# Optimization experiments

Hardware: AMD Instinct MI355X
Metric: run time of the kernel (lower is better)

## Reference

```python
import jax, jax.numpy as jnp
import numpy as np
from jax import lax

S, D, T, FT, FP, H, NH = 100, 30, 40, 512, 3, 64, 4
DH = H // NH

PARAM_SHAPES = {
    'pg_Wih': (S, 3 * H, FP), 'pg_Whh': (S, 3 * H, H), 'pg_bih': (S, 3 * H), 'pg_bhh': (S, 3 * H),
    'pa_W': (S, H, H), 'pa_b': (S, H),
    'tl_Wall': (S, 4 * H, FT), 'tl_bWall': (S, 4 * H), 'tl_Uall': (S, 4 * H, H), 'tl_bUall': (S, 4 * H),
    'tl_Wd': (S, H, H), 'tl_bd': (S, H),
    'ta_W': (S, H, H), 'ta_b': (S, H),
    'sg_Wih': (S, 3 * H, H), 'sg_Whh': (S, 3 * H, H), 'sg_bih': (S, 3 * H), 'sg_bhh': (S, 3 * H),
    'sa_W': (S, H, H), 'sa_b': (S, H),
    'bi_W': (S, H, H, H), 'bi_b': (S, H),
    'bl_W': (S, 2, H), 'bl_b': (S, 2),
    'mha_Wq': (H, H), 'mha_bq': (H,), 'mha_Wk': (H, H), 'mha_bk': (H,),
    'fc_W': (2, H), 'fc_b': (2,),
}


def setup_inputs() -> dict:
    key = jax.random.key(0)
    ks = jax.random.split(key, len(PARAM_SHAPES) + 5)
    inp = {}
    for (name, shp), k in zip(PARAM_SHAPES.items(), ks[:len(PARAM_SHAPES)]):
        inp[name] = jax.random.normal(k, shp, dtype=jnp.float32) * 0.05
    k0, k1, k2, k3, k4 = ks[len(PARAM_SHAPES):]
    inp['text_input'] = jax.random.normal(k0, (S, D, T, FT), dtype=jnp.float32)
    inp['price_input'] = jax.random.normal(k1, (S, D, FP), dtype=jnp.float32)
    inp['timestamps'] = jax.random.uniform(k2, (S, D, T), dtype=jnp.float32)
    inp['label'] = jax.random.randint(k3, (S,), 0, 2, dtype=jnp.int32)
    inp['adj'] = jax.random.randint(k4, (S, S), 0, 2, dtype=jnp.int32)
    inp['train'] = 0
    return inp


def _gru(x_seq, Wih, Whh, bih, bhh):
    # x_seq: [T, Din] -> outs [T, H], h_last [H]
    h0 = jnp.zeros((Whh.shape[1],), x_seq.dtype)
    def step(h, x):
        gx = Wih @ x + bih
        gh = Whh @ h + bhh
        xr, xz, xn = jnp.split(gx, 3)
        hr, hz, hn = jnp.split(gh, 3)
        r = jax.nn.sigmoid(xr + hr)
        z = jax.nn.sigmoid(xz + hz)
        n = jnp.tanh(xn + r * hn)
        h2 = (1.0 - z) * n + z * h
        return h2, h2
    h_last, outs = lax.scan(step, h0, x_seq)
    return outs, h_last


def _timelstm(x_seq, ts, Wall, bWall, Uall, bUall, Wd, bd):
    # x_seq: [T, FT], ts: [T] -> outs [T, H], h_last [H]
    h0 = jnp.zeros((Wd.shape[0],), x_seq.dtype)
    def step(carry, xt):
        h, c = carry
        x, t = xt
        c_s1 = jnp.tanh(Wd @ c + bd)
        c_adj = c - c_s1 + c_s1 * t  # time-decayed cell, as in source
        g = Uall @ h + bUall + Wall @ x + bWall
        f, i, o, ct = jnp.split(g, 4)
        f = jax.nn.sigmoid(f)
        i = jax.nn.sigmoid(i)
        o = jax.nn.sigmoid(o)
        ct = jax.nn.sigmoid(ct)  # sigmoid (not tanh), faithful to source
        c2 = f * c_adj + i * ct
        h2 = o * jnp.tanh(c2)
        return (h2, c2), h2
    (h, c), outs = lax.scan(step, (h0, h0), (x_seq, ts))
    return outs, h


def _attn(outs, h, W, b):
    # Luong-style attention pooling over time: scores_t = outs_t . (W h + b)
    scores = outs @ (W @ h + b)
    return jax.nn.softmax(scores) @ outs


def _stock(price, text, ts, pg_Wih, pg_Whh, pg_bih, pg_bhh, pa_W, pa_b,
           tl_Wall, tl_bWall, tl_Uall, tl_bUall, tl_Wd, tl_bd, ta_W, ta_b,
           sg_Wih, sg_Whh, sg_bih, sg_bhh, sa_W, sa_b, bi_W, bi_b):
    p_outs, p_h = _gru(price, pg_Wih, pg_Whh, pg_bih, pg_bhh)
    x = _attn(p_outs, p_h, pa_W, pa_b)  # [H] price vector
    def day(txt_d, ts_d):
        o, hh = _timelstm(txt_d, ts_d, tl_Wall, tl_bWall, tl_Uall, tl_bUall, tl_Wd, tl_bd)
        return _attn(o, hh, ta_W, ta_b)
    news = jax.vmap(day)(text, ts)  # [D, H]
    s_outs, s_h = _gru(news, sg_Wih, sg_Whh, sg_bih, sg_bhh)
    tvec = _attn(s_outs, s_h, sa_W, sa_b)  # [H] text vector
    return jnp.tanh(jnp.einsum('i,kij,j->k', tvec, bi_W, x) + bi_b)


def _forward(text_input, price_input, timestamps,
             pg_Wih, pg_Whh, pg_bih, pg_bhh, pa_W, pa_b,
             tl_Wall, tl_bWall, tl_Uall, tl_bUall, tl_Wd, tl_bd, ta_W, ta_b,
             sg_Wih, sg_Whh, sg_bih, sg_bhh, sa_W, sa_b, bi_W, bi_b,
             bl_W, bl_b, mha_Wq, mha_bq, mha_Wk, mha_bk, fc_W, fc_b, label):
    feature = jax.vmap(_stock)(price_input, text_input, timestamps,
                               pg_Wih, pg_Whh, pg_bih, pg_bhh, pa_W, pa_b,
                               tl_Wall, tl_bWall, tl_Uall, tl_bUall, tl_Wd, tl_bd, ta_W, ta_b,
                               sg_Wih, sg_Whh, sg_bih, sg_bhh, sa_W, sa_b, bi_W, bi_b)  # [S, H]
    # source bug kept: blending uses the LAST stock's layer on all stocks
    out_1 = jnp.tanh(feature @ bl_W[-1].T + bl_b[-1])  # [S, 2]
    # multi-head self-attention over the stock axis (dropout off: eval mode)
    Q = (feature @ mha_Wq.T + mha_bq).reshape(S, NH, DH)
    K = (feature @ mha_Wk.T + mha_bk).reshape(S, NH, DH)
    V = feature.reshape(S, NH, DH)
    scores = jnp.einsum('shd,thd->hst', Q, K) / (DH ** 0.5)
    a = jax.nn.softmax(scores, axis=-1)
    mh = jnp.einsum('hst,thd->shd', a, V).reshape(S, H)
    x = jax.nn.elu(mh @ fc_W.T + fc_b)  # [S, 2]
    output = jax.nn.softmax(x + out_1, axis=1)
    # faithful to source: CrossEntropyLoss applied to already-softmaxed output
    logp = jax.nn.log_softmax(output, axis=1)
    loss = -jnp.mean(jnp.take_along_axis(logp, label[:, None].astype(jnp.int32), axis=1))
    return loss, output


def reference(text_input, price_input, timestamps,
              pg_Wih, pg_Whh, pg_bih, pg_bhh, pa_W, pa_b,
              tl_Wall, tl_bWall, tl_Uall, tl_bUall, tl_Wd, tl_bd, ta_W, ta_b,
              sg_Wih, sg_Whh, sg_bih, sg_bhh, sa_W, sa_b, bi_W, bi_b,
              bl_W, bl_b, mha_Wq, mha_bq, mha_Wk, mha_bk, fc_W, fc_b,
              label, adj, train):
    del adj, train  # adj feeds dead GraphAttentionLayer in source; eval-mode dropout is identity
    return _forward(text_input, price_input, timestamps,
                    pg_Wih, pg_Whh, pg_bih, pg_bhh, pa_W, pa_b,
                    tl_Wall, tl_bWall, tl_Uall, tl_bUall, tl_Wd, tl_bd, ta_W, ta_b,
                    sg_Wih, sg_Whh, sg_bih, sg_bhh, sa_W, sa_b, bi_W, bi_b,
                    bl_W, bl_b, mha_Wq, mha_bq, mha_Wk, mha_bk, fc_W, fc_b, label)
```

## Files before the change

kernel.cpp:

```cpp
#include <hip/hip_runtime.h>
#include <math.h>

#define S_  100
#define D_  30
#define T_  40
#define FT_ 512
#define FP_ 3
#define H_  64
#define G3  192
#define G4  256
#define M_  (D_*T_)
#define NDY 6

typedef __attribute__((ext_vector_type(8))) short short8_t;
typedef __attribute__((ext_vector_type(4))) short short4_t;
typedef __attribute__((ext_vector_type(4))) float f32x4;

__device__ __forceinline__ float sigm(float x){ return 1.0f/(1.0f+__expf(-x)); }
__device__ __forceinline__ float tanhfast(float x){
  float e = __expf(2.0f*x);
  return 1.0f - 2.0f/(e + 1.0f);
}
__device__ __forceinline__ short f2bf(float f){
  unsigned u = __builtin_bit_cast(unsigned, f);
  u += 0x7FFFu + ((u>>16)&1u);
  return (short)(u>>16);
}
__device__ __forceinline__ float bf2f(unsigned short u){
  unsigned x = ((unsigned)u) << 16;
  return __builtin_bit_cast(float, x);
}
__device__ __forceinline__ short8_t pack8(float4 a, float4 b){
  short8_t o;
  o[0]=f2bf(a.x); o[1]=f2bf(a.y); o[2]=f2bf(a.z); o[3]=f2bf(a.w);
  o[4]=f2bf(b.x); o[5]=f2bf(b.y); o[6]=f2bf(b.z); o[7]=f2bf(b.w);
  return o;
}

__global__ __launch_bounds__(512, 2) void k_gemm_price(
    const float* __restrict__ text, const float* __restrict__ Wall,
    const float* __restrict__ bW, const float* __restrict__ bU,
    unsigned short* __restrict__ GX,
    const float* __restrict__ price, const float* __restrict__ pWih,
    const float* __restrict__ pWhh, const float* __restrict__ pbih,
    const float* __restrict__ pbhh, const float* __restrict__ paW,
    const float* __restrict__ pab, float* __restrict__ xvec)
{
  __shared__ __align__(16) char smem[78848];
  const int tid = threadIdx.x;

  if (blockIdx.x < 1000) {
    const int orig = blockIdx.x;
    const int wg = (orig & 7) * 125 + (orig >> 3);
    const int s  = wg / 10;
    const int mb = wg % 10;
    const int m0 = mb * 128;
    const int lane = tid & 63, wave = tid >> 6;
    const int wm = wave >> 2, wn = wave & 3;
    const int fr = lane & 15, fk = (lane >> 4) * 8;

    float (*As)[128][36] = (float(*)[128][36])smem;
    short (*Bs)[G4][40]  = (short(*)[G4][40])(smem + 36864);
    short (*Es)[264]     = (short(*)[264])smem;
    float* biasL         = (float*)(smem + 77824);

    if (tid < G4) biasL[tid] = bW[s*G4 + tid] + bU[s*G4 + tid];

    const float* X   = text + (size_t)s * ((size_t)M_*FT_);
    const float* Wsl = Wall + (size_t)s * ((size_t)G4*FT_);

    const int rowA = tid >> 2;
    const int colA = (tid & 3) * 8;
    int ar = m0 + rowA; if (ar > M_-1) ar = M_-1;
    const float* aSrc = X + (size_t)ar*FT_ + colA;
    const int rowB = tid >> 1;
    const int colB = (tid & 1) * 16;
    const float* bSrc = Wsl + (size_t)rowB*FT_ + colB;

    f32x4 acc[4][4];
    #pragma unroll
    for (int i=0;i<4;++i)
      #pragma unroll
      for (int j=0;j<4;++j) acc[i][j] = (f32x4)(0.f);

    float4 la0, la1, lb0, lb1, lb2, lb3;
    la0 = *reinterpret_cast<const float4*>(aSrc);
    la1 = *reinterpret_cast<const float4*>(aSrc + 4);
    lb0 = *reinterpret_cast<const float4*>(bSrc);
    lb1 = *reinterpret_cast<const float4*>(bSrc + 4);
    lb2 = *reinterpret_cast<const float4*>(bSrc + 8);
    lb3 = *reinterpret_cast<const float4*>(bSrc + 12);

    for (int kp = 0; kp < 16; ++kp) {
      const int buf = kp & 1;
      *reinterpret_cast<float4*>(&As[buf][rowA][colA])     = la0;
      *reinterpret_cast<float4*>(&As[buf][rowA][colA + 4]) = la1;
      *reinterpret_cast<short8_t*>(&Bs[buf][rowB][colB])     = pack8(lb0, lb1);
      *reinterpret_cast<short8_t*>(&Bs[buf][rowB][colB + 8]) = pack8(lb2, lb3);
      __syncthreads();
      if (kp + 1 < 16) {
        const int ko = (kp + 1) * 32;
        la0 = *reinterpret_cast<const float4*>(aSrc + ko);
        la1 = *reinterpret_cast<const float4*>(aSrc + ko + 4);
        lb0 = *reinterpret_cast<const float4*>(bSrc + ko);
        lb1 = *reinterpret_cast<const float4*>(bSrc + ko + 4);
        lb2 = *reinterpret_cast<const float4*>(bSrc + ko + 8);
        lb3 = *reinterpret_cast<const float4*>(bSrc + ko + 12);
      }
      short8_t bfr[4];
      #pragma unroll
      for (int nt = 0; nt < 4; ++nt)
        bfr[nt] = *reinterpret_cast<const short8_t*>(&Bs[buf][wn*64 + nt*16 + fr][fk]);
      #pragma unroll
      for (int mt = 0; mt < 4; ++mt) {
        float4 x = *reinterpret_cast<const float4*>(&As[buf][wm*64 + mt*16 + fr][fk]);
        float4 y = *reinterpret_cast<const float4*>(&As[buf][wm*64 + mt*16 + fr][fk + 4]);
        short8_t afr = pack8(x, y);
        #pragma unroll
        for (int nt = 0; nt < 4; ++nt)
          acc[mt][nt] = __builtin_amdgcn_mfma_f32_16x16x32_bf16(afr, bfr[nt], acc[mt][nt], 0,0,0);
      }
    }

    __syncthreads();
    {
      const int cl = lane & 15, rh = (lane >> 4) * 4;
      #pragma unroll
      for (int mt = 0; mt < 4; ++mt)
        #pragma unroll
        for (int nt = 0; nt < 4; ++nt) {
          const int cc = wn*64 + nt*16 + cl;
          const float b = biasL[cc];
          #pragma unroll
          for (int r = 0; r < 4; ++r)
            Es[wm*64 + mt*16 + rh + r][cc] = f2bf(acc[mt][nt][r] + b);
        }
    }
    __syncthreads();
    {
      const int r = tid >> 2;
      const int c0 = (tid & 3) * 64;
      const int m = m0 + r;
      if (m < M_) {
        unsigned short* dst = GX + ((size_t)s*M_ + m)*G4 + c0;
        #pragma unroll
        for (int j = 0; j < 8; ++j)
          *reinterpret_cast<short8_t*>(dst + j*8) =
              *reinterpret_cast<const short8_t*>(&Es[r][c0 + j*8]);
      }
    }
    return;
  }

  {
    const int s = blockIdx.x - 1000;
    float* hs   = (float*)smem;
    float (*outsb)[H_+1] = (float(*)[H_+1])(hs + 64);
    float* gsum = hs + 64 + D_*(H_+1);
    float* gxn  = gsum + 128;
    float* ghn  = gxn + 64;
    float (*pt)[H_] = (float(*)[H_])(ghn + 64);
    float* vs   = ghn + 64 + 4*H_;
    float* as_  = vs + 64;
    const int row = tid & 63, q = (tid >> 6) & 3;

    float wih[3]; float whh[64]; float bihr=0.f, bhhr=0.f;
    if (tid < G3) {
      const float* wp = pWih + ((size_t)s*G3 + tid)*FP_;
      wih[0]=wp[0]; wih[1]=wp[1]; wih[2]=wp[2];
      const float* hp = pWhh + ((size_t)s*G3 + tid)*H_;
      #pragma unroll
      for (int j=0;j<64;++j) whh[j]=hp[j];
      bihr = pbih[s*G3+tid]; bhhr = pbhh[s*G3+tid];
    }
    if (tid < H_) hs[tid]=0.f;
    __syncthreads();

    for (int d=0; d<D_; ++d) {
      if (tid < G3) {
        const float* pp = price + ((size_t)s*D_ + d)*FP_;
        float p0=pp[0], p1=pp[1], p2=pp[2];
        float gx = bihr + wih[0]*p0 + wih[1]*p1 + wih[2]*p2;
        float gh = bhhr;
        const float4* h4p = reinterpret_cast<const float4*>(hs);
        #pragma unroll
        for (int j4=0;j4<16;++j4) {
          float4 hv=h4p[j4];
          gh = fmaf(whh[j4*4+0],hv.x,gh); gh = fmaf(whh[j4*4+1],hv.y,gh);
          gh = fmaf(whh[j4*4+2],hv.z,gh); gh = fmaf(whh[j4*4+3],hv.w,gh);
        }
        if (tid < 128) gsum[tid] = gx + gh;
        else { gxn[tid-128] = gx; ghn[tid-128] = gh; }
      }
      __syncthreads();
      if (tid < H_) {
        float r = sigm(gsum[tid]);
        float z = sigm(gsum[64+tid]);
        float n = tanhf(gxn[tid] + r*ghn[tid]);
        float h2 = (1.f-z)*n + z*hs[tid];
        hs[tid]=h2; outsb[d][tid]=h2;
      }
      __syncthreads();
    }
    if (tid < 256) {
      const float* Wp = paW + ((size_t)s*H_ + row)*H_ + q*16;
      float p = 0.f;
      #pragma unroll
      for (int j=0;j<16;++j) p = fmaf(Wp[j], hs[q*16+j], p);
      pt[q][row] = p;
    }
    __syncthreads();
    if (tid < H_) vs[tid] = pt[0][tid]+pt[1][tid]+pt[2][tid]+pt[3][tid] + pab[s*H_+tid];
    __syncthreads();
    if (tid < D_) {
      float sc = 0.f;
      for (int h=0;h<H_;++h) sc = fmaf(outsb[tid][h], vs[h], sc);
      as_[tid] = sc;
    }
    __syncthreads();
    if (tid == 0) {
      float m = -1e30f;
      for (int t=0;t<D_;++t) m = fmaxf(m, as_[t]);
      float sum = 0.f;
      for (int t=0;t<D_;++t) { float e = __expf(as_[t]-m); as_[t]=e; sum += e; }
      float inv = 1.0f/sum;
      for (int t=0;t<D_;++t) as_[t] *= inv;
    }
    __syncthreads();
    if (tid < H_) {
      float acc = 0.f;
      for (int t=0;t<D_;++t) acc = fmaf(as_[t], outsb[t][tid], acc);
      xvec[s*H_+tid] = acc;
    }
  }
}

#define RECUR_STEP(T_CUR, GXU, GXP)                                           \
  {                                                                           \
    {                                                                         \
      const int tpf = ((T_CUR)+1 < T_) ? (T_CUR)+1 : (T_CUR);                 \
      const unsigned short* GXt = GX + ((size_t)s*M_ + d0*T_ + tpf)*G4;       \
      _Pragma("unroll")                                                       \
      for (int it = 0; it < 2; ++it) {                                        \
        int d = it*4 + wave;                                                  \
        if (d < NDY) {                                                        \
          const unsigned short* p = GXt + (size_t)d*T_*G4 + lane;             \
          GXP[it][0]=bf2f(p[0]);   GXP[it][1]=bf2f(p[64]);                    \
          GXP[it][2]=bf2f(p[128]); GXP[it][3]=bf2f(p[192]);                   \
        }                                                                     \
      }                                                                       \
    }                                                                         \
    f32x4 acc1_0=(f32x4)(0.f), acc1_1=(f32x4)(0.f);                           \
    f32x4 acc1_2=(f32x4)(0.f), acc1_3=(f32x4)(0.f);                           \
    f32x4 acc2=(f32x4)(0.f);                                                  \
    _Pragma("unroll")                                                         \
    for (int kw = 0; kw < 2; ++kw) {                                          \
      short8_t bfrag = *reinterpret_cast<const short8_t*>(&Hn[fr][kw*32+fk]); \
      acc1_0 = __builtin_amdgcn_mfma_f32_16x16x32_bf16(ureg[0][kw], bfrag, acc1_0,0,0,0); \
      acc1_1 = __builtin_amdgcn_mfma_f32_16x16x32_bf16(ureg[1][kw], bfrag, acc1_1,0,0,0); \
      acc1_2 = __builtin_amdgcn_mfma_f32_16x16x32_bf16(ureg[2][kw], bfrag, acc1_2,0,0,0); \
      acc1_3 = __builtin_amdgcn_mfma_f32_16x16x32_bf16(ureg[3][kw], bfrag, acc1_3,0,0,0); \
      short8_t cfrag = *reinterpret_cast<const short8_t*>(&Cn[fr][kw*32+fk]); \
      acc2 = __builtin_amdgcn_mfma_f32_16x16x32_bf16(wdreg[kw], cfrag, acc2,0,0,0); \
    }                                                                         \
    *reinterpret_cast<f32x4*>(&G1[l15][wave*64 +  0 + h4]) = acc1_0;          \
    *reinterpret_cast<f32x4*>(&G1[l15][wave*64 + 16 + h4]) = acc1_1;          \
    *reinterpret_cast<f32x4*>(&G1[l15][wave*64 + 32 + h4]) = acc1_2;          \
    *reinterpret_cast<f32x4*>(&G1[l15][wave*64 + 48 + h4]) = acc1_3;          \
    *reinterpret_cast<f32x4*>(&G2l[l15][wave*16 + h4]) = acc2;                \
    __syncthreads();                                                          \
    _Pragma("unroll")                                                         \
    for (int it = 0; it < 2; ++it) {                                          \
      int d = it*4 + wave;                                                    \
      if (d < NDY) {                                                          \
        float gf = G1[d][lane]       + GXU[it][0];                            \
        float gi = G1[d][64 + lane]  + GXU[it][1];                            \
        float go = G1[d][128 + lane] + GXU[it][2];                            \
        float gc = G1[d][192 + lane] + GXU[it][3];                            \
        float f  = sigm(gf), ig = sigm(gi), og = sigm(go), ct = sigm(gc);     \
        float cs1 = tanhfast(G2l[d][lane] + bdl[lane]);                       \
        float tvv = tsl[d][(T_CUR)];                                          \
        float c  = Cf[d][lane];                                               \
        float cadj = c - cs1 + cs1*tvv;                                       \
        float c2 = f*cadj + ig*ct;                                            \
        float h2 = og*tanhfast(c2);                                           \
        Cf[d][lane] = c2; Cn[d][lane] = f2bf(c2); Hn[d][lane] = f2bf(h2);     \
        outs_lds[d][(T_CUR)][lane] = f2bf(h2);                                \
      }                                                                       \
    }                                                                         \
    __syncthreads();                                                          \
  }

__global__ __launch_bounds__(256) void k_recur(
    const unsigned short* __restrict__ GX, const float* __restrict__ Uall,
    const float* __restrict__ Wd, const float* __restrict__ bd,
    const float* __restrict__ ts, const float* __restrict__ taW,
    const float* __restrict__ tab, float* __restrict__ news)
{
  const int bid = blockIdx.x;
  const int s  = bid / 5;
  const int d0 = (bid % 5) * NDY;
  const int tid = threadIdx.x;
  const int lane = tid & 63, wave = tid >> 6;
  const int fr = lane & 15, fk = (lane >> 4) * 8;
  const int l15 = lane & 15, h4 = (lane >> 4) * 4;

  __shared__ float G1[16][260];
  __shared__ float G2l[16][68];
  __shared__ float Cf[8][68];
  __shared__ short Hn[16][72];
  __shared__ short Cn[16][72];
  __shared__ float tsl[NDY][T_];
  __shared__ float bdl[H_], tabl[H_];
  __shared__ float scl[NDY][T_];
  __shared__ short outs_lds[NDY][T_][68];

  for (int e = tid; e < 16*72; e += 256) { (&Hn[0][0])[e] = 0; (&Cn[0][0])[e] = 0; }
  for (int e = tid; e < 8*68; e += 256) (&Cf[0][0])[e] = 0.f;
  for (int e = tid; e < NDY*T_; e += 256)
    (&tsl[0][0])[e] = ts[((size_t)s*D_ + d0)*T_ + e];
  if (tid < H_) { bdl[tid] = bd[s*H_ + tid]; tabl[tid] = tab[s*H_ + tid]; }

  short8_t ureg[4][2], wdreg[2], twreg[2];
  {
    const float* Uf  = Uall + (size_t)s*G4*H_;
    const float* Wdf = Wd   + (size_t)s*H_*H_;
    const float* Twf = taW  + (size_t)s*H_*H_;
    #pragma unroll
    for (int mt = 0; mt < 4; ++mt)
      #pragma unroll
      for (int kw = 0; kw < 2; ++kw) {
        const float* p = Uf + (size_t)(wave*64 + mt*16 + fr)*H_ + kw*32 + fk;
        ureg[mt][kw] = pack8(*reinterpret_cast<const float4*>(p),
                             *reinterpret_cast<const float4*>(p + 4));
      }
    #pragma unroll
    for (int kw = 0; kw < 2; ++kw) {
      const float* p = Wdf + (size_t)(wave*16 + fr)*H_ + kw*32 + fk;
      wdreg[kw] = pack8(*reinterpret_cast<const float4*>(p),
                        *reinterpret_cast<const float4*>(p + 4));
      const float* q = Twf + (size_t)(wave*16 + fr)*H_ + kw*32 + fk;
      twreg[kw] = pack8(*reinterpret_cast<const float4*>(q),
                        *reinterpret_cast<const float4*>(q + 4));
    }
  }
  __syncthreads();

  float gxA[2][4], gxB[2][4];
  {
    const unsigned short* GXt = GX + ((size_t)s*M_ + d0*T_)*G4;
    #pragma unroll
    for (int it = 0; it < 2; ++it) {
      int d = it*4 + wave;
      if (d < NDY) {
        const unsigned short* p = GXt + (size_t)d*T_*G4 + lane;
        gxA[it][0]=bf2f(p[0]);   gxA[it][1]=bf2f(p[64]);
        gxA[it][2]=bf2f(p[128]); gxA[it][3]=bf2f(p[192]);
      }
    }
  }

  for (int t = 0; t < T_; t += 2) {
    RECUR_STEP(t,   gxA, gxB)
    RECUR_STEP(t+1, gxB, gxA)
  }

  {
    f32x4 accv = (f32x4)(0.f);
    #pragma unroll
    for (int kw = 0; kw < 2; ++kw) {
      short8_t hfr = *reinterpret_cast<const short8_t*>(&Hn[fr][kw*32+fk]);
      accv = __builtin_amdgcn_mfma_f32_16x16x32_bf16(twreg[kw], hfr, accv, 0,0,0);
    }
    *reinterpret_cast<f32x4*>(&G2l[l15][wave*16 + h4]) = accv;
  }
  __syncthreads();
  for (int e = tid; e < NDY*H_; e += 256) {
    int d = e >> 6, i = e & 63;
    G2l[d][i] += tabl[i];
  }
  __syncthreads();
  for (int idx = tid; idx < NDY*T_; idx += 256) {
    int d = idx / T_, t = idx % T_;
    float sc = 0.f;
    #pragma unroll 8
    for (int l = 0; l < H_; ++l)
      sc = fmaf(bf2f((unsigned short)outs_lds[d][t][l]), G2l[d][l], sc);
    scl[d][t] = sc;
  }
  __syncthreads();
  if (tid < NDY) {
    float m = -1e30f;
    for (int t = 0; t < T_; ++t) m = fmaxf(m, scl[tid][t]);
    float sum = 0.f;
    for (int t = 0; t < T_; ++t) { float e = __expf(scl[tid][t]-m); scl[tid][t]=e; sum+=e; }
    float inv = 1.f/sum;
    for (int t = 0; t < T_; ++t) scl[tid][t] *= inv;
  }
  __syncthreads();
  {
    const int l = tid & 63, w = tid >> 6;
    for (int d = w; d < NDY; d += 4) {
      float o = 0.f;
      #pragma unroll 8
      for (int t = 0; t < T_; ++t)
        o = fmaf(scl[d][t], bf2f((unsigned short)outs_lds[d][t][l]), o);
      news[((size_t)s*D_ + d0 + d)*H_ + l] = o;
    }
  }
}

__global__ __launch_bounds__(256) void k_rnn(
    const float* __restrict__ news, const float* __restrict__ sWih,
    const float* __restrict__ sWhh, const float* __restrict__ sbih,
    const float* __restrict__ sbhh, const float* __restrict__ saW,
    const float* __restrict__ sab, float* __restrict__ tvecg)
{
  const int s = blockIdx.x;
  const int tid = threadIdx.x;
  const int row = tid & 63, q = tid >> 6;
  __shared__ float xs[H_], hs[H_];
  __shared__ float outsb[D_][H_+1];
  __shared__ float gsum[128], gxn[64], ghn[64];
  __shared__ float pt[4][H_], vs[H_], as_[D_];

  float wih[64]; float whh[64]; float bihr=0.f, bhhr=0.f;
  if (tid < G3) {
    const float* wp = sWih + ((size_t)s*G3 + tid)*H_;
    const float* hp = sWhh + ((size_t)s*G3 + tid)*H_;
    #pragma unroll
    for (int j=0;j<64;++j) { wih[j]=wp[j]; whh[j]=hp[j]; }
    bihr = sbih[s*G3+tid]; bhhr = sbhh[s*G3+tid];
  }
  if (tid < H_) hs[tid]=0.f;
  __syncthreads();

  for (int d=0; d<D_; ++d) {
    if (tid < H_) xs[tid] = news[((size_t)s*D_ + d)*H_ + tid];
    __syncthreads();
    if (tid < G3) {
      float gx = bihr, gh = bhhr;
      const float4* x4 = reinterpret_cast<const float4*>(xs);
      const float4* h4p = reinterpret_cast<const float4*>(hs);
      #pragma unroll
      for (int j4=0;j4<16;++j4) {
        float4 xv=x4[j4]; float4 hv=h4p[j4];
        gx = fmaf(wih[j4*4+0],xv.x,gx); gx = fmaf(wih[j4*4+1],xv.y,gx);
        gx = fmaf(wih[j4*4+2],xv.z,gx); gx = fmaf(wih[j4*4+3],xv.w,gx);
        gh = fmaf(whh[j4*4+0],hv.x,gh); gh = fmaf(whh[j4*4+1],hv.y,gh);
        gh = fmaf(whh[j4*4+2],hv.z,gh); gh = fmaf(whh[j4*4+3],hv.w,gh);
      }
      if (tid < 128) gsum[tid] = gx + gh;
      else { gxn[tid-128] = gx; ghn[tid-128] = gh; }
    }
    __syncthreads();
    if (tid < H_) {
      float r = sigm(gsum[tid]);
      float z = sigm(gsum[64+tid]);
      float n = tanhf(gxn[tid] + r*ghn[tid]);
      float h2 = (1.f-z)*n + z*hs[tid];
      hs[tid]=h2; outsb[d][tid]=h2;
    }
    __syncthreads();
  }

  {
    const float* Wp = saW + ((size_t)s*H_ + row)*H_ + q*16;
    float p = 0.f;
    #pragma unroll
    for (int j=0;j<16;++j) p = fmaf(Wp[j], hs[q*16+j], p);
    pt[q][row] = p;
    __syncthreads();
    if (tid < H_) vs[tid] = pt[0][tid]+pt[1][tid]+pt[2][tid]+pt[3][tid] + sab[s*H_+tid];
    __syncthreads();
    if (tid < D_) {
      float sc = 0.f;
      for (int h=0;h<H_;++h) sc = fmaf(outsb[tid][h], vs[h], sc);
      as_[tid] = sc;
    }
    __syncthreads();
    if (tid == 0) {
      float m = -1e30f;
      for (int t=0;t<D_;++t) m = fmaxf(m, as_[t]);
      float sum = 0.f;
      for (int t=0;t<D_;++t) { float e = __expf(as_[t]-m); as_[t]=e; sum += e; }
      float inv = 1.0f/sum;
      for (int t=0;t<D_;++t) as_[t] *= inv;
    }
    __syncthreads();
    if (tid < H_) {
      float acc = 0.f;
      for (int t=0;t<D_;++t) acc = fmaf(as_[t], outsb[t][tid], acc);
      tvecg[s*H_+tid] = acc;
    }
  }
}

__global__ __launch_bounds__(256) void k_bilin(
    const float* __restrict__ tvec, const float* __restrict__ xvec,
    const float* __restrict__ biW, const float* __restrict__ bib,
    float* __restrict__ feat)
{
  const int s = blockIdx.x >> 2;
  const int k0 = (blockIdx.x & 3) * 16;
  const int tid = threadIdx.x;
  const int lane = tid & 63, w = tid >> 6;
  __shared__ float pmat[H_*H_];
  __shared__ float tl[H_], xl[H_];
  if (tid < H_) { tl[tid] = tvec[s*H_+tid]; xl[tid] = xvec[s*H_+tid]; }
  __syncthreads();
  for (int e = tid; e < H_*H_; e += 256) pmat[e] = tl[e>>6]*xl[e&63];
  __syncthreads();
  const float4* P4 = reinterpret_cast<const float4*>(pmat);
  #pragma unroll
  for (int kk = 0; kk < 4; ++kk) {
    int k = k0 + kk*4 + w;
    const float4* W4 = reinterpret_cast<const float4*>(biW + ((size_t)s*H_ + k)*H_*H_);
    float acc = 0.f;
    #pragma unroll
    for (int r = 0; r < 16; ++r) {
      float4 wv = W4[r*64 + lane];
      float4 pv = P4[r*64 + lane];
      acc += wv.x*pv.x + wv.y*pv.y + wv.z*pv.z + wv.w*pv.w;
    }
    #pragma unroll
    for (int off = 32; off > 0; off >>= 1) acc += __shfl_down(acc, off, 64);
    if (lane == 0) feat[s*H_ + k] = tanhf(acc + bib[s*H_+k]);
  }
}

__global__ __launch_bounds__(128) void k_qk(
    const float* __restrict__ feat, const float* __restrict__ Wq,
    const float* __restrict__ bq, const float* __restrict__ Wk,
    const float* __restrict__ bk, float* __restrict__ Qg,
    float* __restrict__ Kg)
{
  const int s = blockIdx.x;
  const int tid = threadIdx.x;
  __shared__ float fsl[H_];
  if (tid < H_) fsl[tid] = feat[s*H_ + tid];
  __syncthreads();
  const int o = tid & 63;
  const int which = tid >> 6;
  const float* W = which ? Wk : Wq;
  float a = which ? bk[o] : bq[o];
  const float* wr = W + o*H_;
  #pragma unroll 8
  for (int h = 0; h < H_; ++h) a = fmaf(fsl[h], wr[h], a);
  (which ? Kg : Qg)[s*H_ + o] = a;
}

__global__ __launch_bounds__(256) void k_attn(
    const float* __restrict__ feat, const float* __restrict__ Qg,
    const float* __restrict__ Kg, const float* __restrict__ blW,
    const float* __restrict__ blb, const float* __restrict__ fcW,
    const float* __restrict__ fcb, const int* __restrict__ label,
    float* __restrict__ lt, float* __restrict__ dout)
{
  const int s = blockIdx.x;
  const int tid = threadIdx.x;
  __shared__ float Kl[S_][H_];
  __shared__ float Vl[S_][H_];
  __shared__ float ql[H_], mhl[H_], o1l[2];
  __shared__ float scl[4][S_];

  for (int e = tid; e < S_*H_; e += 256) {
    Kl[e>>6][e&63] = Kg[e];
    Vl[e>>6][e&63] = feat[e];
  }
  if (tid < H_) ql[tid] = Qg[s*H_ + tid];
  __syncthreads();

  for (int idx = tid; idx < 4*S_; idx += 256) {
    const int hd = idx / S_, t = idx - hd*S_;
    float sc = 0.f;
    #pragma unroll
    for (int d2 = 0; d2 < 16; ++d2)
      sc = fmaf(ql[hd*16 + d2], Kl[t][hd*16 + d2], sc);
    scl[hd][t] = sc * 0.25f;
  }
  __syncthreads();
  if (tid < 4) {
    float m = -1e30f;
    for (int t = 0; t < S_; ++t) m = fmaxf(m, scl[tid][t]);
    float sum = 0.f;
    for (int t = 0; t < S_; ++t) { float e = __expf(scl[tid][t]-m); scl[tid][t]=e; sum+=e; }
    float inv = 1.f/sum;
    for (int t = 0; t < S_; ++t) scl[tid][t] *= inv;
  }
  if (tid >= 64 && tid < 66) {
    const int c = tid - 64;
    const float* w = blW + ((size_t)(S_-1)*2 + c)*H_;
    float a = blb[(S_-1)*2 + c];
    #pragma unroll 8
    for (int h = 0; h < H_; ++h) a = fmaf(Vl[s][h], w[h], a);
    o1l[c] = tanhf(a);
  }
  __syncthreads();
  if (tid < H_) {
    const int hd = tid >> 4;
    float a = 0.f;
    #pragma unroll 4
    for (int t = 0; t < S_; ++t) a = fmaf(scl[hd][t], Vl[t][tid], a);
    mhl[tid] = a;
  }
  __syncthreads();
  if (tid == 0) {
    float e0 = fcb[0], e1 = fcb[1];
    for (int h = 0; h < H_; ++h) {
      float mv = mhl[h];
      e0 = fmaf(mv, fcW[h], e0);
      e1 = fmaf(mv, fcW[H_ + h], e1);
    }
    float x0 = e0 > 0.f ? e0 : (__expf(e0) - 1.f);
    float x1 = e1 > 0.f ? e1 : (__expf(e1) - 1.f);
    float y0 = x0 + o1l[0], y1 = x1 + o1l[1];
    float mm = fmaxf(y0, y1);
    float p0 = __expf(y0 - mm), p1 = __expf(y1 - mm);
    float is = 1.f / (p0 + p1);
    float out0 = p0 * is, out1 = p1 * is;
    float m2 = fmaxf(out0, out1);
    float lse = m2 + logf(__expf(out0 - m2) + __expf(out1 - m2));
    float ol = (label[s] != 0) ? out1 : out0;
    lt[s] = lse - ol;
    dout[1 + s*2] = out0;
    dout[2 + s*2] = out1;
  }
}

__global__ __launch_bounds__(128) void k_loss(
    const float* __restrict__ lt, float* __restrict__ dout)
{
  const int tid = threadIdx.x;
  __shared__ float buf[128];
  buf[tid] = (tid < S_) ? lt[tid] : 0.f;
  __syncthreads();
  #pragma unroll
  for (int off = 64; off > 0; off >>= 1) {
    if (tid < off) buf[tid] += buf[tid + off];
    __syncthreads();
  }
  if (tid == 0) dout[0] = buf[0] * (1.0f / (float)S_);
}

extern "C" void kernel_launch(void* const* d_in, const int* in_sizes, int n_in,
                              void* d_out, int out_size, void* d_ws, size_t ws_size,
                              hipStream_t stream) {
  const float* pg_Wih  = (const float*)d_in[0];
  const float* pg_Whh  = (const float*)d_in[1];
  const float* pg_bih  = (const float*)d_in[2];
  const float* pg_bhh  = (const float*)d_in[3];
  const float* pa_W    = (const float*)d_in[4];
  const float* pa_b    = (const float*)d_in[5];
  const float* tl_Wall = (const float*)d_in[6];
  const float* tl_bWall= (const float*)d_in[7];
  const float* tl_Uall = (const float*)d_in[8];
  const float* tl_bUall= (const float*)d_in[9];
  const float* tl_Wd   = (const float*)d_in[10];
  const float* tl_bd   = (const float*)d_in[11];
  const float* ta_W    = (const float*)d_in[12];
  const float* ta_b    = (const float*)d_in[13];
  const float* sg_Wih  = (const float*)d_in[14];
  const float* sg_Whh  = (const float*)d_in[15];
  const float* sg_bih  = (const float*)d_in[16];
  const float* sg_bhh  = (const float*)d_in[17];
  const float* sa_W    = (const float*)d_in[18];
  const float* sa_b    = (const float*)d_in[19];
  const float* bi_W    = (const float*)d_in[20];
  const float* bi_b    = (const float*)d_in[21];
  const float* bl_W    = (const float*)d_in[22];
  const float* bl_b    = (const float*)d_in[23];
  const float* mha_Wq  = (const float*)d_in[24];
  const float* mha_bq  = (const float*)d_in[25];
  const float* mha_Wk  = (const float*)d_in[26];
  const float* mha_bk  = (const float*)d_in[27];
  const float* fc_W    = (const float*)d_in[28];
  const float* fc_b    = (const float*)d_in[29];
  const float* text    = (const float*)d_in[30];
  const float* price   = (const float*)d_in[31];
  const float* tstamps = (const float*)d_in[32];
  const int*   label   = (const int*)d_in[33];
  (void)in_sizes; (void)n_in; (void)out_size; (void)ws_size;

  unsigned short* GXbf = (unsigned short*)d_ws;
  float* news   = (float*)(GXbf + (size_t)S_*M_*G4);
  float* xvec   = news + (size_t)S_*D_*H_;
  float* feat   = xvec + (size_t)S_*H_;
  float* Qg     = feat + (size_t)S_*H_;
  float* Kg     = Qg   + (size_t)S_*H_;
  float* ltb    = Kg   + (size_t)S_*H_;
  float* tvecg  = ltb  + 128;
  float* dout   = (float*)d_out;

  k_gemm_price<<<1100, 512, 0, stream>>>(text, tl_Wall, tl_bWall, tl_bUall, GXbf,
                                         price, pg_Wih, pg_Whh, pg_bih, pg_bhh,
                                         pa_W, pa_b, xvec);
  k_recur<<<5*S_, 256, 0, stream>>>(GXbf, tl_Uall, tl_Wd, tl_bd, tstamps, ta_W, ta_b, news);
  k_rnn<<<S_, 256, 0, stream>>>(news, sg_Wih, sg_Whh, sg_bih, sg_bhh, sa_W, sa_b, tvecg);
  k_bilin<<<4*S_, 256, 0, stream>>>(tvecg, xvec, bi_W, bi_b, feat);
  k_qk<<<S_, 128, 0, stream>>>(feat, mha_Wq, mha_bq, mha_Wk, mha_bk, Qg, Kg);
  k_attn<<<S_, 256, 0, stream>>>(feat, Qg, Kg, bl_W, bl_b, fc_W, fc_b, label, ltb, dout);
  k_loss<<<1, 128, 0, stream>>>(ltb, dout);
}
```

Measured before the change: 283.3 us.

## Store A tile as bf16 in LDS and prefetch two K-panels ahead

The A operand is now packed to bf16 once when it is stored to LDS, instead of being held as fp32 in LDS and repacked by every wave before each MFMA. This halves A-tile LDS traffic and shrinks the LDS footprint. The global-load prefetch is also deepened to two register sets, so loads for panel k+2 are in flight while panel k is computed, with the loop fully unrolled. The extra register set raises VGPR pressure under the 512x2 launch bounds and could cause spills.

```diff
diff --git a/kernel.cpp b/kernel.cpp
--- a/kernel.cpp
+++ b/kernel.cpp
@@ -37,6 +37,34 @@
   return o;
 }
 
+#define GEMM_PANEL(BUF, SET, KPN)                                             \
+  {                                                                           \
+    *reinterpret_cast<short8_t*>(&As[BUF][rowA][colA]) = pack8(SET##a0, SET##a1); \
+    *reinterpret_cast<short8_t*>(&Bs[BUF][rowB][colB])     = pack8(SET##b0, SET##b1); \
+    *reinterpret_cast<short8_t*>(&Bs[BUF][rowB][colB + 8]) = pack8(SET##b2, SET##b3); \
+    __syncthreads();                                                          \
+    if ((KPN) < 16) {                                                         \
+      const int ko = (KPN) * 32;                                              \
+      SET##a0 = *reinterpret_cast<const float4*>(aSrc + ko);                  \
+      SET##a1 = *reinterpret_cast<const float4*>(aSrc + ko + 4);              \
+      SET##b0 = *reinterpret_cast<const float4*>(bSrc + ko);                  \
+      SET##b1 = *reinterpret_cast<const float4*>(bSrc + ko + 4);              \
+      SET##b2 = *reinterpret_cast<const float4*>(bSrc + ko + 8);              \
+      SET##b3 = *reinterpret_cast<const float4*>(bSrc + ko + 12);             \
+    }                                                                         \
+    short8_t bfr[4];                                                          \
+    _Pragma("unroll")                                                         \
+    for (int nt = 0; nt < 4; ++nt)                                            \
+      bfr[nt] = *reinterpret_cast<const short8_t*>(&Bs[BUF][wn*64 + nt*16 + fr][fk]); \
+    _Pragma("unroll")                                                         \
+    for (int mt = 0; mt < 4; ++mt) {                                          \
+      short8_t afr = *reinterpret_cast<const short8_t*>(&As[BUF][wm*64 + mt*16 + fr][fk]); \
+      _Pragma("unroll")                                                       \
+      for (int nt = 0; nt < 4; ++nt)                                          \
+        acc[mt][nt] = __builtin_amdgcn_mfma_f32_16x16x32_bf16(afr, bfr[nt], acc[mt][nt], 0,0,0); \
+    }                                                                         \
+  }
+
 __global__ __launch_bounds__(512, 2) void k_gemm_price(
     const float* __restrict__ text, const float* __restrict__ Wall,
     const float* __restrict__ bW, const float* __restrict__ bU,
@@ -46,7 +74,7 @@
     const float* __restrict__ pbhh, const float* __restrict__ paW,
     const float* __restrict__ pab, float* __restrict__ xvec)
 {
-  __shared__ __align__(16) char smem[78848];
+  __shared__ __align__(16) char smem[68608];
   const int tid = threadIdx.x;
 
   if (blockIdx.x < 1000) {
@@ -59,10 +87,10 @@
     const int wm = wave >> 2, wn = wave & 3;
     const int fr = lane & 15, fk = (lane >> 4) * 8;
 
-    float (*As)[128][36] = (float(*)[128][36])smem;
-    short (*Bs)[G4][40]  = (short(*)[G4][40])(smem + 36864);
+    short (*As)[128][40] = (short(*)[128][40])smem;
+    short (*Bs)[G4][40]  = (short(*)[G4][40])(smem + 20480);
     short (*Es)[264]     = (short(*)[264])smem;
-    float* biasL         = (float*)(smem + 77824);
+    float* biasL         = (float*)(smem + 67584);
 
     if (tid < G4) biasL[tid] = bW[s*G4 + tid] + bU[s*G4 + tid];
 
@@ -83,43 +111,25 @@
       #pragma unroll
       for (int j=0;j<4;++j) acc[i][j] = (f32x4)(0.f);
 
-    float4 la0, la1, lb0, lb1, lb2, lb3;
-    la0 = *reinterpret_cast<const float4*>(aSrc);
-    la1 = *reinterpret_cast<const float4*>(aSrc + 4);
-    lb0 = *reinterpret_cast<const float4*>(bSrc);
-    lb1 = *reinterpret_cast<const float4*>(bSrc + 4);
-    lb2 = *reinterpret_cast<const float4*>(bSrc + 8);
-    lb3 = *reinterpret_cast<const float4*>(bSrc + 12);
-
-    for (int kp = 0; kp < 16; ++kp) {
-      const int buf = kp & 1;
-      *reinterpret_cast<float4*>(&As[buf][rowA][colA])     = la0;
-      *reinterpret_cast<float4*>(&As[buf][rowA][colA + 4]) = la1;
-      *reinterpret_cast<short8_t*>(&Bs[buf][rowB][colB])     = pack8(lb0, lb1);
-      *reinterpret_cast<short8_t*>(&Bs[buf][rowB][colB + 8]) = pack8(lb2, lb3);
-      __syncthreads();
-      if (kp + 1 < 16) {
-        const int ko = (kp + 1) * 32;
-        la0 = *reinterpret_cast<const float4*>(aSrc + ko);
-        la1 = *reinterpret_cast<const float4*>(aSrc + ko + 4);
-        lb0 = *reinterpret_cast<const float4*>(bSrc + ko);
-        lb1 = *reinterpret_cast<const float4*>(bSrc + ko + 4);
-        lb2 = *reinterpret_cast<const float4*>(bSrc + ko + 8);
-        lb3 = *reinterpret_cast<const float4*>(bSrc + ko + 12);
-      }
-      short8_t bfr[4];
-      #pragma unroll
-      for (int nt = 0; nt < 4; ++nt)
-        bfr[nt] = *reinterpret_cast<const short8_t*>(&Bs[buf][wn*64 + nt*16 + fr][fk]);
-      #pragma unroll
-      for (int mt = 0; mt < 4; ++mt) {
-        float4 x = *reinterpret_cast<const float4*>(&As[buf][wm*64 + mt*16 + fr][fk]);
-        float4 y = *reinterpret_cast<const float4*>(&As[buf][wm*64 + mt*16 + fr][fk + 4]);
-        short8_t afr = pack8(x, y);
-        #pragma unroll
-        for (int nt = 0; nt < 4; ++nt)
-          acc[mt][nt] = __builtin_amdgcn_mfma_f32_16x16x32_bf16(afr, bfr[nt], acc[mt][nt], 0,0,0);
-      }
+    float4 Xa0, Xa1, Xb0, Xb1, Xb2, Xb3;
+    float4 Ya0, Ya1, Yb0, Yb1, Yb2, Yb3;
+    Xa0 = *reinterpret_cast<const float4*>(aSrc);
+    Xa1 = *reinterpret_cast<const float4*>(aSrc + 4);
+    Xb0 = *reinterpret_cast<const float4*>(bSrc);
+    Xb1 = *reinterpret_cast<const float4*>(bSrc + 4);
+    Xb2 = *reinterpret_cast<const float4*>(bSrc + 8);
+    Xb3 = *reinterpret_cast<const float4*>(bSrc + 12);
+    Ya0 = *reinterpret_cast<const float4*>(aSrc + 32);
+    Ya1 = *reinterpret_cast<const float4*>(aSrc + 36);
+    Yb0 = *reinterpret_cast<const float4*>(bSrc + 32);
+    Yb1 = *reinterpret_cast<const float4*>(bSrc + 36);
+    Yb2 = *reinterpret_cast<const float4*>(bSrc + 40);
+    Yb3 = *reinterpret_cast<const float4*>(bSrc + 44);
+
+    #pragma unroll
+    for (int kp = 0; kp < 16; kp += 2) {
+      GEMM_PANEL(0, X, kp + 2)
+      GEMM_PANEL(1, Y, kp + 3)
     }
 
     __syncthreads();
```

New measurement: 316.4 us. +11.7%, slower.
